# Kernel tuning notes

Hardware: AMD Instinct MI355X
Metric: run time of the kernel (lower is better)

Reference implementation:

```python
import jax, jax.numpy as jnp
import numpy as np

N_NODES = 100000
N_EDGES = 3200000
DIM = 64
N_LAYERS = 3


def setup_inputs() -> dict:
    key = jax.random.key(0)
    ks = jax.random.split(key, 8)
    x = jax.random.normal(ks[0], (N_NODES, DIM), dtype=jnp.float32)
    a = jax.random.uniform(ks[1], (N_EDGES,), dtype=jnp.float32)
    # weights stored as [in_dim, out_dim] so layer op is h @ W + b
    W1s = jax.random.normal(ks[2], (N_LAYERS, DIM, DIM), dtype=jnp.float32) * (1.0 / np.sqrt(DIM))
    b1s = jnp.zeros((N_LAYERS, DIM), dtype=jnp.float32)
    W2s = jax.random.normal(ks[3], (N_LAYERS, DIM, DIM), dtype=jnp.float32) * (1.0 / np.sqrt(DIM))
    b2s = jnp.zeros((N_LAYERS, DIM), dtype=jnp.float32)
    src = jax.random.randint(ks[4], (N_EDGES,), 0, N_NODES, dtype=jnp.int32)
    dst = jax.random.randint(ks[5], (N_EDGES,), 0, N_NODES, dtype=jnp.int32)
    return {"x": x, "a": a, "W1s": W1s, "b1s": b1s, "W2s": W2s, "b2s": b2s,
            "src": src, "dst": dst}


def reference(x, a, W1s, b1s, W2s, b2s, src, dst):
    """KGAT forward (eval mode, dropouts=0, normalize=False, full-graph blocks).

    Per layer: h_n[v] = sum_{e:(u->v)} a_e * h[u]
               h <- LeakyReLU((h + h_n) @ W1 + b1) + LeakyReLU((h * h_n) @ W2 + b2)
    Output: concat([x, h_1, h_2, h_3], axis=1) -> [N, 4*DIM]
    """
    n = x.shape[0]
    h = x
    embs = [x]
    for l in range(N_LAYERS):
        msg = h[src] * a[:, None]                      # [E, d] gather + edge scale
        h_n = jax.ops.segment_sum(msg, dst, num_segments=n)  # [N, d] scatter-add
        h = (jax.nn.leaky_relu((h + h_n) @ W1s[l] + b1s[l], 0.01)
             + jax.nn.leaky_relu((h * h_n) @ W2s[l] + b2s[l], 0.01))
        embs.append(h)
    return jnp.concatenate(embs, axis=1)
```

## Files before the change

kernel.cpp:

```cpp
#include <hip/hip_runtime.h>
#include <hip/hip_bf16.h>

#define N_NODES 100000
#define N_EDGES 3200000
#define DIM 64
#define OUT_COLS 256
#define BUCKET_SHIFT 8
#define NBUCK ((N_NODES + 255) / 256)
#define TILE 4096
#define NTILEBLK ((N_EDGES + TILE - 1) / TILE)
#define NODE_TILES ((N_NODES + 63) / 64)
#define WFRAG_PER_LAYER (2 * 2 * 4 * 64 * 8)

typedef __attribute__((ext_vector_type(8))) short short8;
typedef __attribute__((ext_vector_type(4))) float f32x4;

__device__ __forceinline__ unsigned short f2bf(float f) {
    __hip_bfloat16 b = __float2bfloat16(f);
    unsigned short u;
    __builtin_memcpy(&u, &b, 2);
    return u;
}
__device__ __forceinline__ unsigned int pkbf(float a, float b) {
    return (unsigned int)f2bf(a) | ((unsigned int)f2bf(b) << 16);
}
__device__ __forceinline__ float bflo(unsigned int p) { return __uint_as_float(p << 16); }
__device__ __forceinline__ float bfhi(unsigned int p) { return __uint_as_float(p & 0xFFFF0000u); }

__global__ void init_kernel(const float* __restrict__ x,
                            float* __restrict__ h,
                            unsigned short* __restrict__ h_bf,
                            float* __restrict__ out) {
    int i = blockIdx.x * blockDim.x + threadIdx.x;
    const int total = N_NODES * DIM / 4;
    if (i < total) {
        float4 v = ((const float4*)x)[i];
        ((float4*)h)[i] = v;
        int elem = i * 4;
        int node = elem >> 6;
        int c    = elem & 63;
        *(float4*)&out[node * OUT_COLS + c] = v;
        unsigned int lo = pkbf(v.x, v.y);
        unsigned int hi = pkbf(v.z, v.w);
        *(uint2*)&h_bf[elem] = make_uint2(lo, hi);
    }
}

__global__ __launch_bounds__(256) void wprep_kernel(const float* __restrict__ W1s,
                                                    const float* __restrict__ W2s,
                                                    unsigned short* __restrict__ wfrag) {
    int idx = blockIdx.x * 256 + threadIdx.x;
    if (idx >= 3 * WFRAG_PER_LAYER) return;
    int j     = idx & 7;
    int lane  = (idx >> 3) & 63;
    int ct    = (idx >> 9) & 3;
    int kt    = (idx >> 11) & 1;
    int mat   = (idx >> 12) & 1;
    int layer = idx >> 13;
    int k   = kt * 32 + (lane >> 4) * 8 + j;
    int col = ct * 16 + (lane & 15);
    const float* W = (mat ? W2s : W1s) + (size_t)layer * DIM * DIM;
    wfrag[idx] = f2bf(W[k * DIM + col]);
}

__global__ __launch_bounds__(256) void count_kernel(const int* __restrict__ dst,
                                                    int* __restrict__ mat) {
    __shared__ int lc[NBUCK];
    for (int b = threadIdx.x; b < NBUCK; b += 256) lc[b] = 0;
    __syncthreads();
    const int base = blockIdx.x * TILE;
#pragma unroll
    for (int k = 0; k < TILE / 256; ++k) {
        int e = base + k * 256 + threadIdx.x;
        if (e < N_EDGES) atomicAdd(&lc[((unsigned)dst[e]) >> BUCKET_SHIFT], 1);
    }
    __syncthreads();
    int* row = mat + (size_t)blockIdx.x * NBUCK;
    for (int b = threadIdx.x; b < NBUCK; b += 256) row[b] = lc[b];
}

__global__ __launch_bounds__(256) void scan2_kernel(int* __restrict__ mat,
                                                    int* __restrict__ bucket_count) {
    const int b = blockIdx.x;
    const int t = threadIdx.x;
    int cpre[4];
    int s = 0;
#pragma unroll
    for (int j = 0; j < 4; ++j) {
        int blk = t * 4 + j;
        cpre[j] = s;
        int v = (blk < NTILEBLK) ? mat[(size_t)blk * NBUCK + b] : 0;
        s += v;
    }
    __shared__ int ss[256];
    ss[t] = s;
    __syncthreads();
    for (int off = 1; off < 256; off <<= 1) {
        int u = (t >= off) ? ss[t - off] : 0;
        __syncthreads();
        ss[t] += u;
        __syncthreads();
    }
    int excl = ss[t] - s;
#pragma unroll
    for (int j = 0; j < 4; ++j) {
        int blk = t * 4 + j;
        if (blk < NTILEBLK) mat[(size_t)blk * NBUCK + b] = excl + cpre[j];
    }
    if (t == 255) bucket_count[b] = ss[255];
}

__global__ __launch_bounds__(512) void bucket_scan_kernel(const int* __restrict__ bucket_count,
                                                          int* __restrict__ bucket_base,
                                                          int* __restrict__ offsets) {
    __shared__ int s[512];
    const int t = threadIdx.x;
    int v = (t < NBUCK) ? bucket_count[t] : 0;
    s[t] = v;
    __syncthreads();
    for (int off = 1; off < 512; off <<= 1) {
        int u = (t >= off) ? s[t - off] : 0;
        __syncthreads();
        s[t] += u;
        __syncthreads();
    }
    if (t < NBUCK) bucket_base[t] = s[t] - v;
    if (t == 0) offsets[N_NODES] = N_EDGES;
}

__global__ __launch_bounds__(256) void binA_kernel(const int* __restrict__ src,
                                                   const int* __restrict__ dst,
                                                   const float* __restrict__ a,
                                                   const int* __restrict__ bucket_base,
                                                   const int* __restrict__ mat,
                                                   int2* __restrict__ temp) {
    __shared__ int lcount[NBUCK];
    __shared__ int lscan[512];
    __shared__ int lgbase[NBUCK];
    __shared__ int2 stage[TILE];
    __shared__ unsigned short sbuck[TILE];

    const int t = threadIdx.x;
    const int base = blockIdx.x * TILE;

    for (int b = t; b < NBUCK; b += 256) lcount[b] = 0;
    __syncthreads();

    int dv[TILE / 256], rk[TILE / 256];
#pragma unroll
    for (int k = 0; k < TILE / 256; ++k) {
        int e = base + k * 256 + t;
        dv[k] = 0; rk[k] = 0;
        if (e < N_EDGES) {
            int d = dst[e];
            dv[k] = d;
            rk[k] = atomicAdd(&lcount[((unsigned)d) >> BUCKET_SHIFT], 1);
        }
    }
    __syncthreads();

    lscan[t]       = (t < NBUCK) ? lcount[t] : 0;
    lscan[t + 256] = (t + 256 < NBUCK) ? lcount[t + 256] : 0;
    __syncthreads();
    for (int off = 1; off < 512; off <<= 1) {
        int u0 = (t >= off) ? lscan[t - off] : 0;
        int u1 = ((t + 256) >= off) ? lscan[t + 256 - off] : 0;
        __syncthreads();
        lscan[t] += u0;
        lscan[t + 256] += u1;
        __syncthreads();
    }
    {
        const int* row = mat + (size_t)blockIdx.x * NBUCK;
        for (int b = t; b < NBUCK; b += 256) {
            int excl = lscan[b] - lcount[b];
            lgbase[b] = bucket_base[b] + row[b] - excl;
        }
    }
    __syncthreads();

#pragma unroll
    for (int k = 0; k < TILE / 256; ++k) {
        int e = base + k * 256 + t;
        if (e < N_EDGES) {
            int d = dv[k];
            int b = ((unsigned)d) >> BUCKET_SHIFT;
            int slot = (lscan[b] - lcount[b]) + rk[k];
            stage[slot] = make_int2(src[e] | ((d & 255) << 24), __float_as_int(a[e]));
            sbuck[slot] = (unsigned short)b;
        }
    }
    __syncthreads();

    const int cntT = min(TILE, N_EDGES - base);
    for (int i = t; i < cntT; i += 256) {
        temp[lgbase[sbuck[i]] + i] = stage[i];
    }
}

__global__ __launch_bounds__(256) void binB_kernel(const int2* __restrict__ temp,
                                                   const int* __restrict__ bucket_base,
                                                   const int* __restrict__ bucket_count,
                                                   int* __restrict__ offsets,
                                                   int2* __restrict__ edges) {
    const int b = blockIdx.x;
    const int node0 = b << BUCKET_SHIFT;
    const int nodes = min(256, N_NODES - node0);
    const int beg = bucket_base[b];
    const int cnt = bucket_count[b];
    const int t = threadIdx.x;

    __shared__ int ncount[256];
    __shared__ int ssc[256];
    __shared__ int ncur[256];
    ncount[t] = 0;
    __syncthreads();
    for (int i = t; i < cnt; i += 256) {
        unsigned w0 = (unsigned)temp[beg + i].x;
        atomicAdd(&ncount[w0 >> 24], 1);
    }
    __syncthreads();
    int v = ncount[t];
    ssc[t] = v;
    __syncthreads();
    for (int off = 1; off < 256; off <<= 1) {
        int u = (t >= off) ? ssc[t - off] : 0;
        __syncthreads();
        ssc[t] += u;
        __syncthreads();
    }
    int excl = ssc[t] - v;
    if (t < nodes) offsets[node0 + t] = beg + excl;
    ncur[t] = beg + excl;
    __syncthreads();
    for (int i = t; i < cnt; i += 256) {
        int2 r = temp[beg + i];
        int loc = ((unsigned)r.x) >> 24;
        int pos = atomicAdd(&ncur[loc], 1);
        edges[pos] = make_int2(r.x & 0xFFFFFF, r.y);
    }
}

__global__ __launch_bounds__(256) void gather_kernel(
        const unsigned short* __restrict__ h_bf,
        const int2* __restrict__ edges,
        const int* __restrict__ offsets,
        float* __restrict__ hn) {
    const int lane   = threadIdx.x & 63;
    const int half   = lane >> 5;
    const int sub    = lane & 31;
    const int waveid = (blockIdx.x * blockDim.x + threadIdx.x) >> 6;
    const int node   = waveid * 2 + half;
    if (node >= N_NODES) return;

    const int beg = offsets[node];
    const int end = offsets[node + 1];
    const int col2 = sub * 2;

    float al0 = 0.f, al1 = 0.f, al2 = 0.f, al3 = 0.f;
    float ah0 = 0.f, ah1 = 0.f, ah2 = 0.f, ah3 = 0.f;
    int i = beg;
    for (; i + 4 <= end; i += 4) {
        int2 e0 = edges[i + 0];
        int2 e1 = edges[i + 1];
        int2 e2 = edges[i + 2];
        int2 e3 = edges[i + 3];
        unsigned int p0 = *(const unsigned int*)&h_bf[(size_t)e0.x * DIM + col2];
        unsigned int p1 = *(const unsigned int*)&h_bf[(size_t)e1.x * DIM + col2];
        unsigned int p2 = *(const unsigned int*)&h_bf[(size_t)e2.x * DIM + col2];
        unsigned int p3 = *(const unsigned int*)&h_bf[(size_t)e3.x * DIM + col2];
        float w0 = __int_as_float(e0.y);
        float w1 = __int_as_float(e1.y);
        float w2 = __int_as_float(e2.y);
        float w3 = __int_as_float(e3.y);
        al0 = fmaf(w0, bflo(p0), al0);  ah0 = fmaf(w0, bfhi(p0), ah0);
        al1 = fmaf(w1, bflo(p1), al1);  ah1 = fmaf(w1, bfhi(p1), ah1);
        al2 = fmaf(w2, bflo(p2), al2);  ah2 = fmaf(w2, bfhi(p2), ah2);
        al3 = fmaf(w3, bflo(p3), al3);  ah3 = fmaf(w3, bfhi(p3), ah3);
    }
    for (; i < end; ++i) {
        int2 e = edges[i];
        unsigned int p = *(const unsigned int*)&h_bf[(size_t)e.x * DIM + col2];
        float w = __int_as_float(e.y);
        al0 = fmaf(w, bflo(p), al0);
        ah0 = fmaf(w, bfhi(p), ah0);
    }
    float lo = (al0 + al1) + (al2 + al3);
    float hi = (ah0 + ah1) + (ah2 + ah3);
    *(float2*)&hn[(size_t)node * DIM + col2] = make_float2(lo, hi);
}

__global__ __launch_bounds__(256) void update_kernel(
        float* __restrict__ h,
        unsigned short* __restrict__ h_bf,
        const float* __restrict__ hn,
        const unsigned short* __restrict__ wfrag,
        const float* __restrict__ b1,
        const float* __restrict__ b2,
        float* __restrict__ out,
        int out_col_base) {
    __shared__ unsigned short t1s[64 * 64];
    __shared__ unsigned short t2s[64 * 64];

    const int t    = threadIdx.x;
    const int lane = t & 63;
    const int wid  = t >> 6;
    const int node0 = blockIdx.x * 64;

    short8 w1f[2][4], w2f[2][4];
#pragma unroll
    for (int kt = 0; kt < 2; ++kt)
#pragma unroll
        for (int ct = 0; ct < 4; ++ct) {
            w1f[kt][ct] = *(const short8*)(wfrag + (((0 * 2 + kt) * 4 + ct) * 64 + lane) * 8);
            w2f[kt][ct] = *(const short8*)(wfrag + (((1 * 2 + kt) * 4 + ct) * 64 + lane) * 8);
        }
    float bb1[4], bb2[4];
#pragma unroll
    for (int ct = 0; ct < 4; ++ct) {
        bb1[ct] = b1[ct * 16 + (lane & 15)];
        bb2[ct] = b2[ct * 16 + (lane & 15)];
    }

    {
        const int row = t >> 2;
        const int kc  = (t & 3) * 16;
        const int node = node0 + row;
        float tv1[16], tv2[16];
        if (node < N_NODES) {
            const float4* hp  = (const float4*)&h [(size_t)node * DIM + kc];
            const float4* hnp = (const float4*)&hn[(size_t)node * DIM + kc];
#pragma unroll
            for (int i = 0; i < 4; ++i) {
                float4 a = hp[i];
                float4 b = hnp[i];
                tv1[i * 4 + 0] = a.x + b.x;  tv2[i * 4 + 0] = a.x * b.x;
                tv1[i * 4 + 1] = a.y + b.y;  tv2[i * 4 + 1] = a.y * b.y;
                tv1[i * 4 + 2] = a.z + b.z;  tv2[i * 4 + 2] = a.z * b.z;
                tv1[i * 4 + 3] = a.w + b.w;  tv2[i * 4 + 3] = a.w * b.w;
            }
        } else {
#pragma unroll
            for (int i = 0; i < 16; ++i) { tv1[i] = 0.f; tv2[i] = 0.f; }
        }
        const int sw = (row & 7) << 4;
        const int base = row * 128 + (t & 3) * 32;
        uint4 q;
        q.x = pkbf(tv1[0], tv1[1]);  q.y = pkbf(tv1[2], tv1[3]);
        q.z = pkbf(tv1[4], tv1[5]);  q.w = pkbf(tv1[6], tv1[7]);
        *(uint4*)((char*)t1s + ((base) ^ sw)) = q;
        q.x = pkbf(tv1[8], tv1[9]);  q.y = pkbf(tv1[10], tv1[11]);
        q.z = pkbf(tv1[12], tv1[13]); q.w = pkbf(tv1[14], tv1[15]);
        *(uint4*)((char*)t1s + ((base + 16) ^ sw)) = q;
        q.x = pkbf(tv2[0], tv2[1]);  q.y = pkbf(tv2[2], tv2[3]);
        q.z = pkbf(tv2[4], tv2[5]);  q.w = pkbf(tv2[6], tv2[7]);
        *(uint4*)((char*)t2s + ((base) ^ sw)) = q;
        q.x = pkbf(tv2[8], tv2[9]);  q.y = pkbf(tv2[10], tv2[11]);
        q.z = pkbf(tv2[12], tv2[13]); q.w = pkbf(tv2[14], tv2[15]);
        *(uint4*)((char*)t2s + ((base + 16) ^ sw)) = q;
    }
    __syncthreads();

    const int arow = wid * 16 + (lane & 15);
    const int asw  = (arow & 7) << 4;
    short8 a1[2], a2[2];
#pragma unroll
    for (int kt = 0; kt < 2; ++kt) {
        int ab = (arow * 128 + kt * 64 + ((lane >> 4) << 4)) ^ asw;
        a1[kt] = *(const short8*)((const char*)t1s + ab);
        a2[kt] = *(const short8*)((const char*)t2s + ab);
    }

    f32x4 acc1[4], acc2[4];
#pragma unroll
    for (int ct = 0; ct < 4; ++ct) {
        acc1[ct] = (f32x4){bb1[ct], bb1[ct], bb1[ct], bb1[ct]};
        acc2[ct] = (f32x4){bb2[ct], bb2[ct], bb2[ct], bb2[ct]};
    }
#pragma unroll
    for (int ct = 0; ct < 4; ++ct) {
        acc1[ct] = __builtin_amdgcn_mfma_f32_16x16x32_bf16(a1[0], w1f[0][ct], acc1[ct], 0, 0, 0);
        acc1[ct] = __builtin_amdgcn_mfma_f32_16x16x32_bf16(a1[1], w1f[1][ct], acc1[ct], 0, 0, 0);
        acc2[ct] = __builtin_amdgcn_mfma_f32_16x16x32_bf16(a2[0], w2f[0][ct], acc2[ct], 0, 0, 0);
        acc2[ct] = __builtin_amdgcn_mfma_f32_16x16x32_bf16(a2[1], w2f[1][ct], acc2[ct], 0, 0, 0);
    }

#pragma unroll
    for (int ct = 0; ct < 4; ++ct) {
        const int col = ct * 16 + (lane & 15);
#pragma unroll
        for (int r = 0; r < 4; ++r) {
            const int grow = node0 + wid * 16 + (lane >> 4) * 4 + r;
            if (grow < N_NODES) {
                float v1 = acc1[ct][r]; v1 = v1 > 0.f ? v1 : 0.01f * v1;
                float v2 = acc2[ct][r]; v2 = v2 > 0.f ? v2 : 0.01f * v2;
                float hnew = v1 + v2;
                h[(size_t)grow * DIM + col] = hnew;
                h_bf[(size_t)grow * DIM + col] = f2bf(hnew);
                out[(size_t)grow * OUT_COLS + out_col_base + col] = hnew;
            }
        }
    }
}

extern "C" void kernel_launch(void* const* d_in, const int* in_sizes, int n_in,
                              void* d_out, int out_size, void* d_ws, size_t ws_size,
                              hipStream_t stream) {
    const float* x   = (const float*)d_in[0];
    const float* a   = (const float*)d_in[1];
    const float* W1s = (const float*)d_in[2];
    const float* b1s = (const float*)d_in[3];
    const float* W2s = (const float*)d_in[4];
    const float* b2s = (const float*)d_in[5];
    const int*   src = (const int*)d_in[6];
    const int*   dst = (const int*)d_in[7];
    float* out = (float*)d_out;

    float* h  = (float*)d_ws;
    float* hn = h + (size_t)N_NODES * DIM;
    unsigned short* h_bf = (unsigned short*)(hn + (size_t)N_NODES * DIM);
    int* offsets       = (int*)(h_bf + (size_t)N_NODES * DIM);
    int* bucket_count  = offsets + N_NODES + 1;
    int* bucket_base   = bucket_count + NBUCK;
    uintptr_t p = (uintptr_t)(bucket_base + NBUCK);
    p = (p + 15) & ~(uintptr_t)15;
    int2* edges = (int2*)p;
    int2* temp  = (int2*)hn;
    uintptr_t p2 = (uintptr_t)(edges + N_EDGES);
    p2 = (p2 + 15) & ~(uintptr_t)15;
    unsigned short* wfrag = (unsigned short*)p2;
    uintptr_t p3 = (uintptr_t)(wfrag + 3 * WFRAG_PER_LAYER);
    p3 = (p3 + 15) & ~(uintptr_t)15;
    int* mat = (int*)p3;

    {
        int total = N_NODES * DIM / 4;
        init_kernel<<<(total + 255) / 256, 256, 0, stream>>>(x, h, h_bf, out);
    }

    wprep_kernel<<<(3 * WFRAG_PER_LAYER + 255) / 256, 256, 0, stream>>>(W1s, W2s, wfrag);

    count_kernel<<<NTILEBLK, 256, 0, stream>>>(dst, mat);
    scan2_kernel<<<NBUCK, 256, 0, stream>>>(mat, bucket_count);
    bucket_scan_kernel<<<1, 512, 0, stream>>>(bucket_count, bucket_base, offsets);
    binA_kernel<<<NTILEBLK, 256, 0, stream>>>(src, dst, a, bucket_base, mat, temp);
    binB_kernel<<<NBUCK, 256, 0, stream>>>(temp, bucket_base, bucket_count, offsets, edges);

    for (int l = 0; l < 3; ++l) {
        int waves = (N_NODES + 1) / 2;
        int blocks = (waves * 64 + 255) / 256;
        gather_kernel<<<blocks, 256, 0, stream>>>(h_bf, edges, offsets, hn);
        update_kernel<<<NODE_TILES, 256, 0, stream>>>(
            h, h_bf, hn,
            wfrag + (size_t)l * WFRAG_PER_LAYER,
            b1s + (size_t)l * DIM,
            b2s + (size_t)l * DIM,
            out, (l + 1) * DIM);
    }
}
```

Measured before the change: 520.9 us.

## Fuse neighbor gather into the MFMA update kernel with double-buffered bf16 features

Merges the per-layer gather kernel and the update kernel into one kernel. Each block now aggregates neighbor messages for its 64 nodes and writes h+h_n and h*h_n straight into shared memory before the MFMA matmuls. This removes the fp32 h_n round trip through global memory and one launch per layer. The bf16 feature copy is double-buffered (ping-pong) so blocks can write new features while other blocks still read the old ones. The trade-off is less parallelism: about 6k waves, each aggregating 8 nodes in sequence, against about 50k independent gather waves before. That may weaken memory-latency hiding and load balance.

```diff
diff --git a/kernel.cpp b/kernel.cpp
--- a/kernel.cpp
+++ b/kernel.cpp
@@ -241,59 +241,12 @@
     }
 }
 
-__global__ __launch_bounds__(256) void gather_kernel(
-        const unsigned short* __restrict__ h_bf,
+__global__ __launch_bounds__(256) void gup_kernel(
+        const unsigned short* __restrict__ hbf_in,
         const int2* __restrict__ edges,
         const int* __restrict__ offsets,
-        float* __restrict__ hn) {
-    const int lane   = threadIdx.x & 63;
-    const int half   = lane >> 5;
-    const int sub    = lane & 31;
-    const int waveid = (blockIdx.x * blockDim.x + threadIdx.x) >> 6;
-    const int node   = waveid * 2 + half;
-    if (node >= N_NODES) return;
-
-    const int beg = offsets[node];
-    const int end = offsets[node + 1];
-    const int col2 = sub * 2;
-
-    float al0 = 0.f, al1 = 0.f, al2 = 0.f, al3 = 0.f;
-    float ah0 = 0.f, ah1 = 0.f, ah2 = 0.f, ah3 = 0.f;
-    int i = beg;
-    for (; i + 4 <= end; i += 4) {
-        int2 e0 = edges[i + 0];
-        int2 e1 = edges[i + 1];
-        int2 e2 = edges[i + 2];
-        int2 e3 = edges[i + 3];
-        unsigned int p0 = *(const unsigned int*)&h_bf[(size_t)e0.x * DIM + col2];
-        unsigned int p1 = *(const unsigned int*)&h_bf[(size_t)e1.x * DIM + col2];
-        unsigned int p2 = *(const unsigned int*)&h_bf[(size_t)e2.x * DIM + col2];
-        unsigned int p3 = *(const unsigned int*)&h_bf[(size_t)e3.x * DIM + col2];
-        float w0 = __int_as_float(e0.y);
-        float w1 = __int_as_float(e1.y);
-        float w2 = __int_as_float(e2.y);
-        float w3 = __int_as_float(e3.y);
-        al0 = fmaf(w0, bflo(p0), al0);  ah0 = fmaf(w0, bfhi(p0), ah0);
-        al1 = fmaf(w1, bflo(p1), al1);  ah1 = fmaf(w1, bfhi(p1), ah1);
-        al2 = fmaf(w2, bflo(p2), al2);  ah2 = fmaf(w2, bfhi(p2), ah2);
-        al3 = fmaf(w3, bflo(p3), al3);  ah3 = fmaf(w3, bfhi(p3), ah3);
-    }
-    for (; i < end; ++i) {
-        int2 e = edges[i];
-        unsigned int p = *(const unsigned int*)&h_bf[(size_t)e.x * DIM + col2];
-        float w = __int_as_float(e.y);
-        al0 = fmaf(w, bflo(p), al0);
-        ah0 = fmaf(w, bfhi(p), ah0);
-    }
-    float lo = (al0 + al1) + (al2 + al3);
-    float hi = (ah0 + ah1) + (ah2 + ah3);
-    *(float2*)&hn[(size_t)node * DIM + col2] = make_float2(lo, hi);
-}
-
-__global__ __launch_bounds__(256) void update_kernel(
         float* __restrict__ h,
-        unsigned short* __restrict__ h_bf,
-        const float* __restrict__ hn,
+        unsigned short* __restrict__ hbf_out,
         const unsigned short* __restrict__ wfrag,
         const float* __restrict__ b1,
         const float* __restrict__ b2,
@@ -306,6 +259,57 @@
     const int lane = t & 63;
     const int wid  = t >> 6;
     const int node0 = blockIdx.x * 64;
+    const int hw   = t >> 5;
+    const int sub  = t & 31;
+    const int c2   = sub * 2;
+
+#pragma unroll 1
+    for (int j = 0; j < 8; ++j) {
+        const int row  = hw * 8 + j;
+        const int node = node0 + row;
+        float t1lo = 0.f, t1hi = 0.f, t2lo = 0.f, t2hi = 0.f;
+        if (node < N_NODES) {
+            const int beg = offsets[node];
+            const int end = offsets[node + 1];
+            float al0 = 0.f, al1 = 0.f, al2 = 0.f, al3 = 0.f;
+            float ah0 = 0.f, ah1 = 0.f, ah2 = 0.f, ah3 = 0.f;
+            int i = beg;
+            for (; i + 4 <= end; i += 4) {
+                int2 e0 = edges[i + 0];
+                int2 e1 = edges[i + 1];
+                int2 e2 = edges[i + 2];
+                int2 e3 = edges[i + 3];
+                unsigned p0 = *(const unsigned*)&hbf_in[(size_t)e0.x * DIM + c2];
+                unsigned p1 = *(const unsigned*)&hbf_in[(size_t)e1.x * DIM + c2];
+                unsigned p2 = *(const unsigned*)&hbf_in[(size_t)e2.x * DIM + c2];
+                unsigned p3 = *(const unsigned*)&hbf_in[(size_t)e3.x * DIM + c2];
+                float w0 = __int_as_float(e0.y);
+                float w1 = __int_as_float(e1.y);
+                float w2 = __int_as_float(e2.y);
+                float w3 = __int_as_float(e3.y);
+                al0 = fmaf(w0, bflo(p0), al0);  ah0 = fmaf(w0, bfhi(p0), ah0);
+                al1 = fmaf(w1, bflo(p1), al1);  ah1 = fmaf(w1, bfhi(p1), ah1);
+                al2 = fmaf(w2, bflo(p2), al2);  ah2 = fmaf(w2, bfhi(p2), ah2);
+                al3 = fmaf(w3, bflo(p3), al3);  ah3 = fmaf(w3, bfhi(p3), ah3);
+            }
+            for (; i < end; ++i) {
+                int2 e = edges[i];
+                unsigned p = *(const unsigned*)&hbf_in[(size_t)e.x * DIM + c2];
+                float w = __int_as_float(e.y);
+                al0 = fmaf(w, bflo(p), al0);
+                ah0 = fmaf(w, bfhi(p), ah0);
+            }
+            float lo = (al0 + al1) + (al2 + al3);
+            float hi = (ah0 + ah1) + (ah2 + ah3);
+            float2 hv = *(const float2*)&h[(size_t)node * DIM + c2];
+            t1lo = hv.x + lo;  t1hi = hv.y + hi;
+            t2lo = hv.x * lo;  t2hi = hv.y * hi;
+        }
+        const int sw = (row & 7) << 4;
+        const int bo = (row * 128 + sub * 4) ^ sw;
+        *(unsigned*)((char*)t1s + bo) = pkbf(t1lo, t1hi);
+        *(unsigned*)((char*)t2s + bo) = pkbf(t2lo, t2hi);
+    }
 
     short8 w1f[2][4], w2f[2][4];
 #pragma unroll
@@ -320,44 +324,6 @@
     for (int ct = 0; ct < 4; ++ct) {
         bb1[ct] = b1[ct * 16 + (lane & 15)];
         bb2[ct] = b2[ct * 16 + (lane & 15)];
-    }
-
-    {
-        const int row = t >> 2;
-        const int kc  = (t & 3) * 16;
-        const int node = node0 + row;
-        float tv1[16], tv2[16];
-        if (node < N_NODES) {
-            const float4* hp  = (const float4*)&h [(size_t)node * DIM + kc];
-            const float4* hnp = (const float4*)&hn[(size_t)node * DIM + kc];
-#pragma unroll
-            for (int i = 0; i < 4; ++i) {
-                float4 a = hp[i];
-                float4 b = hnp[i];
-                tv1[i * 4 + 0] = a.x + b.x;  tv2[i * 4 + 0] = a.x * b.x;
-                tv1[i * 4 + 1] = a.y + b.y;  tv2[i * 4 + 1] = a.y * b.y;
-                tv1[i * 4 + 2] = a.z + b.z;  tv2[i * 4 + 2] = a.z * b.z;
-                tv1[i * 4 + 3] = a.w + b.w;  tv2[i * 4 + 3] = a.w * b.w;
-            }
-        } else {
-#pragma unroll
-            for (int i = 0; i < 16; ++i) { tv1[i] = 0.f; tv2[i] = 0.f; }
-        }
-        const int sw = (row & 7) << 4;
-        const int base = row * 128 + (t & 3) * 32;
-        uint4 q;
-        q.x = pkbf(tv1[0], tv1[1]);  q.y = pkbf(tv1[2], tv1[3]);
-        q.z = pkbf(tv1[4], tv1[5]);  q.w = pkbf(tv1[6], tv1[7]);
-        *(uint4*)((char*)t1s + ((base) ^ sw)) = q;
-        q.x = pkbf(tv1[8], tv1[9]);  q.y = pkbf(tv1[10], tv1[11]);
-        q.z = pkbf(tv1[12], tv1[13]); q.w = pkbf(tv1[14], tv1[15]);
-        *(uint4*)((char*)t1s + ((base + 16) ^ sw)) = q;
-        q.x = pkbf(tv2[0], tv2[1]);  q.y = pkbf(tv2[2], tv2[3]);
-        q.z = pkbf(tv2[4], tv2[5]);  q.w = pkbf(tv2[6], tv2[7]);
-        *(uint4*)((char*)t2s + ((base) ^ sw)) = q;
-        q.x = pkbf(tv2[8], tv2[9]);  q.y = pkbf(tv2[10], tv2[11]);
-        q.z = pkbf(tv2[12], tv2[13]); q.w = pkbf(tv2[14], tv2[15]);
-        *(uint4*)((char*)t2s + ((base + 16) ^ sw)) = q;
     }
     __syncthreads();
 
@@ -396,7 +362,7 @@
                 float v2 = acc2[ct][r]; v2 = v2 > 0.f ? v2 : 0.01f * v2;
                 float hnew = v1 + v2;
                 h[(size_t)grow * DIM + col] = hnew;
-                h_bf[(size_t)grow * DIM + col] = f2bf(hnew);
+                hbf_out[(size_t)grow * DIM + col] = f2bf(hnew);
                 out[(size_t)grow * OUT_COLS + out_col_base + col] = hnew;
             }
         }
@@ -416,17 +382,15 @@
     const int*   dst = (const int*)d_in[7];
     float* out = (float*)d_out;
 
-    float* h  = (float*)d_ws;
-    float* hn = h + (size_t)N_NODES * DIM;
-    unsigned short* h_bf = (unsigned short*)(hn + (size_t)N_NODES * DIM);
-    int* offsets       = (int*)(h_bf + (size_t)N_NODES * DIM);
-    int* bucket_count  = offsets + N_NODES + 1;
-    int* bucket_base   = bucket_count + NBUCK;
-    uintptr_t p = (uintptr_t)(bucket_base + NBUCK);
-    p = (p + 15) & ~(uintptr_t)15;
-    int2* edges = (int2*)p;
-    int2* temp  = (int2*)hn;
-    uintptr_t p2 = (uintptr_t)(edges + N_EDGES);
+    float* h = (float*)d_ws;
+    int2* edges = (int2*)(h + (size_t)N_NODES * DIM);
+    int2* temp  = edges + (size_t)N_EDGES;
+    unsigned short* hbf0 = (unsigned short*)(temp + (size_t)N_EDGES);
+    unsigned short* hbf1 = hbf0 + (size_t)N_NODES * DIM;
+    int* offsets = (int*)(hbf1 + (size_t)N_NODES * DIM);
+    int* bucket_count = offsets + N_NODES + 1;
+    int* bucket_base  = bucket_count + NBUCK;
+    uintptr_t p2 = (uintptr_t)(bucket_base + NBUCK);
     p2 = (p2 + 15) & ~(uintptr_t)15;
     unsigned short* wfrag = (unsigned short*)p2;
     uintptr_t p3 = (uintptr_t)(wfrag + 3 * WFRAG_PER_LAYER);
@@ -435,7 +399,7 @@
 
     {
         int total = N_NODES * DIM / 4;
-        init_kernel<<<(total + 255) / 256, 256, 0, stream>>>(x, h, h_bf, out);
+        init_kernel<<<(total + 255) / 256, 256, 0, stream>>>(x, h, hbf0, out);
     }
 
     wprep_kernel<<<(3 * WFRAG_PER_LAYER + 255) / 256, 256, 0, stream>>>(W1s, W2s, wfrag);
@@ -446,15 +410,18 @@
     binA_kernel<<<NTILEBLK, 256, 0, stream>>>(src, dst, a, bucket_base, mat, temp);
     binB_kernel<<<NBUCK, 256, 0, stream>>>(temp, bucket_base, bucket_count, offsets, edges);
 
+    const unsigned short* hin = hbf0;
+    unsigned short* hout = hbf1;
     for (int l = 0; l < 3; ++l) {
-        int waves = (N_NODES + 1) / 2;
-        int blocks = (waves * 64 + 255) / 256;
-        gather_kernel<<<blocks, 256, 0, stream>>>(h_bf, edges, offsets, hn);
-        update_kernel<<<NODE_TILES, 256, 0, stream>>>(
-            h, h_bf, hn,
+        gup_kernel<<<NODE_TILES, 256, 0, stream>>>(
+            hin, edges, offsets,
+            h, hout,
             wfrag + (size_t)l * WFRAG_PER_LAYER,
             b1s + (size_t)l * DIM,
             b2s + (size_t)l * DIM,
             out, (l + 1) * DIM);
-    }
-}
+        unsigned short* tmp = hout;
+        hout = (unsigned short*)hin;
+        hin = tmp;
+    }
+}
```

Result: slower. 673.7 us (+29.3%).
